# Kernel optimization log

Measured on AMD Instinct MI355X. Metric: run time of the kernel, lower is better.

Reference implementation:

```python
import jax, jax.numpy as jnp
import numpy as np

K = -1.0          # manifold curvature (hyperbolic / Poincare ball)
SK = 1.0          # sqrt(|K|)
EPS = 1e-7


def _artan_k(x):
    # inverse of tan_k for K<0: artanh(sqrt(|K|) x)/sqrt(|K|)
    return jnp.arctanh(jnp.clip(SK * x, -1.0 + EPS, 1.0 - EPS)) / SK


def _tan_k(x):
    return jnp.tanh(SK * x) / SK


def _norm(x):
    return jnp.maximum(jnp.linalg.norm(x, axis=-1, keepdims=True), 1e-15)


def mobius_add(x, y):
    xy = jnp.sum(x * y, -1, keepdims=True)
    x2 = jnp.sum(x * x, -1, keepdims=True)
    y2 = jnp.sum(y * y, -1, keepdims=True)
    num = (1.0 - 2.0 * K * xy - K * y2) * x + (1.0 + K * x2) * y
    den = 1.0 - 2.0 * K * xy + K * K * x2 * y2
    return num / jnp.maximum(den, 1e-15)


def mobius_scalar_mul(r, x):
    # r may be scalar or (n,1) per-row scalar
    xn = _norm(x)
    return _tan_k(r * _artan_k(xn)) * x / xn


def mobius_matvec(W, x):
    # geoopt convention: (m @ x) per point -> x @ W^T
    xn = _norm(x)
    mx = x @ W.T
    mxn = _norm(mx)
    return _tan_k(mxn / xn * _artan_k(xn)) * mx / mxn


def lambda_x(x):
    # conformal factor lambda_x = 2 / (1 + K |x|^2); returns shape (...,)
    return 2.0 / jnp.maximum(1.0 + K * jnp.sum(x * x, -1), 1e-10)


def expmap0(u):
    un = _norm(u)
    return _tan_k(un) * u / un


def logmap0(y):
    yn = _norm(y)
    return _artan_k(yn) * y / yn


def kappa_left_multiply(A, X):
    # Vectorized per-node weighted gyro-midpoint + mobius scalar mul.
    # out_i = (sum_j A_ij) otimes gyromidpoint(X, weights=A_i)
    gamma = lambda_x(X)                              # (n,)
    denom = A @ (gamma - 1.0)                        # (n,)
    denom = jnp.where(jnp.abs(denom) < 1e-10, 1e-10, denom)
    nom = A @ (gamma[:, None] * X)                   # (n,d)
    two_mean = nom / denom[:, None]
    m = mobius_scalar_mul(0.5, two_mean)             # gyromidpoint
    return mobius_scalar_mul(jnp.sum(A, axis=1, keepdims=True), m)


def setup_inputs() -> dict:
    key = jax.random.key(0)
    k1, k2, k3, k4, k5 = jax.random.split(key, 5)
    n, d, c = 8192, 256, 16
    # node embeddings on the Poincare ball (small norm, well inside the ball)
    X = 0.01 * jax.random.normal(k1, (n, d), jnp.float32)
    # dense normalized adjacency (positive weights, row sums O(1))
    A_hat = jax.random.uniform(k2, (n, n), dtype=jnp.float32) / n
    W = jax.random.uniform(k3, (d, d), dtype=jnp.float32)        # torch.rand init
    W_logits = jax.random.uniform(k4, (d, c), dtype=jnp.float32)
    # p_ks = expmap0(rand), scaled for numerical stability
    p_ks = expmap0(0.05 * jax.random.uniform(k5, (c, d), dtype=jnp.float32))
    return {"X": X, "A_hat": A_hat, "W": W, "W_logits": W_logits, "p_ks": p_ks}


def reference(X, A_hat, W, W_logits, p_ks):
    # hidden kappa-GCN layer
    XW = mobius_matvec(W, X)                          # (n,d)
    AXW = kappa_left_multiply(A_hat, XW)              # (n,d)
    H1 = expmap0(jax.nn.relu(logmap0(AXW)))           # manifold.apply(relu)
    # hyperbolic logits (kappa != 0 branch, K<0 -> asinh)
    z = mobius_add(-p_ks[None, :, :], H1[:, None, :]) # (n,k,d)
    z_n = jnp.linalg.norm(z, axis=-1)                 # (n,k)
    a_n = jnp.maximum(jnp.linalg.norm(W_logits, axis=0), 1e-15)  # (k,)
    za = jnp.einsum('nkd,dk->nk', z, W_logits)
    den = jnp.maximum(1.0 + K * z_n * z_n, 1e-10) * a_n
    dist = jnp.arcsinh(2.0 * SK * za / den)
    lam = lambda_x(p_ks)                              # (k,)
    logits = (lam * a_n / SK) * dist                  # (n,k)
    return A_hat @ logits
```

## Files before the change

### kernel.cpp

```cpp
#include <hip/hip_runtime.h>
#include <math.h>

#define Nn 8192
#define Dd 256
#define Cc 16

#define OFF_BP   4194304u
#define OFF_LOG  5242880u
#define OFF_G1B  5373952u
#define OFF_DEN  5378048u
#define OFF_RS   5410816u
#define OFF_KC   5443584u
#define OFF_LB   5443648u
#define WS_FLOATS 5509184u

typedef short vshort8 __attribute__((ext_vector_type(8)));
typedef float vfloat4 __attribute__((ext_vector_type(4)));

#define AS1 __attribute__((address_space(1)))
#define AS3 __attribute__((address_space(3)))

__device__ __forceinline__ float clip1(float x) {
    return fminf(fmaxf(x, -1.0f + 1e-7f), 1.0f - 1e-7f);
}

__device__ __forceinline__ unsigned short f2bf(float f) {
    unsigned int u = __float_as_uint(f);
    u += 0x7fff + ((u >> 16) & 1);
    return (unsigned short)(u >> 16);
}

__device__ __forceinline__ float bf2f(unsigned short b) {
    return __uint_as_float(((unsigned int)b) << 16);
}

__device__ __forceinline__ float waveReduce(float v) {
    #pragma unroll
    for (int off = 32; off; off >>= 1) v += __shfl_down(v, off);
    return v;
}

__device__ __forceinline__ float blockReduceBcast(float v, float* red) {
    int t = threadIdx.x, w = t >> 6, l = t & 63;
    v = waveReduce(v);
    if (l == 0) red[w] = v;
    __syncthreads();
    if (t == 0) red[0] = red[0] + red[1] + red[2] + red[3];
    __syncthreads();
    float r = red[0];
    __syncthreads();
    return r;
}

__global__ __launch_bounds__(256) void k_consts(const float* __restrict__ Wl,
                                                const float* __restrict__ Pk,
                                                float* __restrict__ kc) {
    __shared__ float red[8];
    int t = threadIdx.x, k = blockIdx.x;
    float pv = Pk[k * Dd + t];
    float wv = Wl[t * Cc + k];
    float p2 = blockReduceBcast(pv * pv, red);
    float pw = blockReduceBcast(pv * wv, red);
    float w2 = blockReduceBcast(wv * wv, red);
    if (t == 0) {
        float an  = fmaxf(sqrtf(w2), 1e-15f);
        float lam = 2.0f / fmaxf(1.0f - p2, 1e-10f);
        kc[k * 4 + 0] = p2; kc[k * 4 + 1] = pw;
        kc[k * 4 + 2] = an; kc[k * 4 + 3] = lam;
    }
}

__global__ __launch_bounds__(256) void k_front(const float* __restrict__ X,
                                               const float* __restrict__ W,
                                               unsigned short* __restrict__ Bp,
                                               unsigned short* __restrict__ g1b) {
    __shared__ __align__(16) unsigned short Xs[32][256];
    __shared__ __align__(16) unsigned short Gs[32][258];
    __shared__ float xs2[32];
    __shared__ float scal[32];
    __shared__ float red4[32][4];

    const int t = threadIdx.x;
    const int l = t & 63, w = t >> 6;
    const int ll = l & 15, kh = l >> 4;
    const int m0 = blockIdx.x * 32;
    const int ar = t >> 3, aq = t & 7;
    const int c0 = w * 64;

    float x2p = 0.f;
    #pragma unroll
    for (int tc = 0; tc < 4; ++tc) {
        const float* xp = &X[(size_t)(m0 + ar) * Dd + tc * 64 + aq * 8];
        vfloat4 v0 = *(const vfloat4*)xp;
        vfloat4 v1 = *(const vfloat4*)(xp + 4);
        vshort8 o;
        #pragma unroll
        for (int e = 0; e < 4; ++e) {
            x2p += v0[e] * v0[e] + v1[e] * v1[e];
            o[e] = (short)f2bf(v0[e]);
            o[e + 4] = (short)f2bf(v1[e]);
        }
        int byte = (tc * 64 + aq * 8) * 2;
        *(vshort8*)((char*)&Xs[ar][0] + (byte ^ ((ar & 7) << 4))) = o;
    }
    x2p += __shfl_xor(x2p, 1); x2p += __shfl_xor(x2p, 2); x2p += __shfl_xor(x2p, 4);
    if (aq == 0) xs2[ar] = x2p;
    __syncthreads();

    vfloat4 acc[2][4];
    #pragma unroll
    for (int mi = 0; mi < 2; ++mi)
        #pragma unroll
        for (int ni = 0; ni < 4; ++ni)
            acc[mi][ni] = (vfloat4){0.f, 0.f, 0.f, 0.f};
    #pragma unroll
    for (int tc = 0; tc < 4; ++tc) {
        vshort8 bf[8];
        #pragma unroll
        for (int ni = 0; ni < 4; ++ni)
            #pragma unroll
            for (int kk = 0; kk < 2; ++kk) {
                const float* wp = &W[(size_t)(c0 + ni * 16 + ll) * Dd
                                     + tc * 64 + kh * 8 + kk * 32];
                vfloat4 b0 = *(const vfloat4*)wp;
                vfloat4 b1 = *(const vfloat4*)(wp + 4);
                vshort8 o;
                #pragma unroll
                for (int e = 0; e < 4; ++e) {
                    o[e] = (short)f2bf(b0[e]);
                    o[e + 4] = (short)f2bf(b1[e]);
                }
                bf[ni * 2 + kk] = o;
            }
        #pragma unroll
        for (int kk = 0; kk < 2; ++kk) {
            int byte = (tc * 64 + kh * 8 + kk * 32) * 2;
            vshort8 af[2];
            #pragma unroll
            for (int mi = 0; mi < 2; ++mi) {
                int row = mi * 16 + ll;
                af[mi] = *(const vshort8*)((const char*)&Xs[row][0]
                                           + (byte ^ ((row & 7) << 4)));
            }
            #pragma unroll
            for (int mi = 0; mi < 2; ++mi)
                #pragma unroll
                for (int ni = 0; ni < 4; ++ni)
                    acc[mi][ni] = __builtin_amdgcn_mfma_f32_16x16x32_bf16(
                        af[mi], bf[ni * 2 + kk], acc[mi][ni], 0, 0, 0);
        }
    }

    #pragma unroll
    for (int mi = 0; mi < 2; ++mi)
        #pragma unroll
        for (int j = 0; j < 4; ++j) {
            float p = 0.f;
            #pragma unroll
            for (int ni = 0; ni < 4; ++ni)
                p += acc[mi][ni][j] * acc[mi][ni][j];
            p += __shfl_xor(p, 1); p += __shfl_xor(p, 2);
            p += __shfl_xor(p, 4); p += __shfl_xor(p, 8);
            if (ll == 0) red4[mi * 16 + kh * 4 + j][w] = p;
        }
    __syncthreads();

    if (t < 32) {
        float mx2 = red4[t][0] + red4[t][1] + red4[t][2] + red4[t][3];
        float xn = fmaxf(sqrtf(xs2[t]), 1e-15f);
        float mxn = fmaxf(sqrtf(mx2), 1e-15f);
        float s = tanhf(mxn / xn * atanhf(clip1(xn))) / mxn;
        float xw2 = s * s * mx2;
        float gamma = 2.0f / fmaxf(1.0f - xw2, 1e-10f);
        scal[t] = gamma * s;
        g1b[m0 + t] = f2bf(gamma - 1.0f);
    }
    __syncthreads();

    #pragma unroll
    for (int mi = 0; mi < 2; ++mi)
        #pragma unroll
        for (int ni = 0; ni < 4; ++ni) {
            int row = mi * 16 + kh * 4;
            int col = c0 + ni * 16 + ll;
            #pragma unroll
            for (int j = 0; j < 4; ++j)
                Gs[row + j][col] = f2bf(scal[row + j] * acc[mi][ni][j]);
        }
    __syncthreads();

    const int s = blockIdx.x;
    #pragma unroll
    for (int pass = 0; pass < 4; ++pass) {
        int c = pass * 256 + t;
        int gni = c >> 6, lc = c & 63;
        int col = (gni >> 2) * 64 + (gni & 3) * 16 + (lc & 15);
        int kh8 = (lc >> 4) * 8;
        vshort8 o;
        #pragma unroll
        for (int e = 0; e < 8; ++e) o[e] = (short)Gs[kh8 + e][col];
        *(vshort8*)&Bp[((size_t)(s * 16 + gni) * 64 + lc) * 8] = o;
    }
}

__device__ __forceinline__ void g2_issueB(const unsigned short* __restrict__ Bp,
        unsigned short (&BsB)[16][512], int splt, int slab, int w, int l) {
    #pragma unroll
    for (int ni = 0; ni < 4; ++ni)
        __builtin_amdgcn_global_load_lds(
            (const AS1 unsigned int*)
                (Bp + ((size_t)((splt * 64 + slab) * 16 + w * 4 + ni) * 512) + l * 8),
            (AS3 unsigned int*)&BsB[w * 4 + ni][0], 16, 0, 0);
}

__device__ __forceinline__ void g2_loadA(const float* __restrict__ Abase,
                                         int tile, float (&a8)[8]) {
    const vfloat4* p = (const vfloat4*)(Abase + tile * 32);
    *(vfloat4*)&a8[0] = p[0];
    *(vfloat4*)&a8[4] = p[1];
}

__device__ __forceinline__ void g2_stage(unsigned short (&AsB)[2048],
        const unsigned short* g1s, const float (&a8)[8],
        int tile, int rowst, int kq, float& dacc, float& racc) {
    vshort8 gv = *(const vshort8*)&g1s[tile * 32 + kq * 8];
    vshort8 o;
    #pragma unroll
    for (int e = 0; e < 8; ++e) {
        float av = a8[e];
        o[e] = (short)f2bf(av);
        dacc += av * bf2f((unsigned short)gv[e]);
        racc += av;
    }
    *(vshort8*)((char*)&AsB[0] + rowst * 64 + ((kq * 16) ^ ((rowst & 3) << 4))) = o;
}

__device__ __forceinline__ void g2_mfma(const unsigned short (&AsB)[2048],
        const unsigned short (&BsB)[16][512], int w, int kh, int ll15, int l,
        vfloat4 (&acc)[4][4]) {
    vshort8 bf[4], af[4];
    #pragma unroll
    for (int ni = 0; ni < 4; ++ni)
        bf[ni] = *(const vshort8*)&BsB[w * 4 + ni][l * 8];
    #pragma unroll
    for (int mi = 0; mi < 4; ++mi) {
        int row = mi * 16 + ll15;
        af[mi] = *(const vshort8*)((const char*)&AsB[0]
                  + row * 64 + ((kh * 16) ^ ((row & 3) << 4)));
    }
    __builtin_amdgcn_s_setprio(1);
    #pragma unroll
    for (int mi = 0; mi < 4; ++mi)
        #pragma unroll
        for (int ni = 0; ni < 4; ++ni)
            acc[mi][ni] = __builtin_amdgcn_mfma_f32_16x16x32_bf16(
                af[mi], bf[ni], acc[mi][ni], 0, 0, 0);
    __builtin_amdgcn_s_setprio(0);
}

__global__ __launch_bounds__(256, 2) void k_gemm1_mfma(
        const float* __restrict__ A,
        const unsigned short* __restrict__ Bp,
        const unsigned short* __restrict__ g1b,
        unsigned short* __restrict__ Pp,
        float* __restrict__ denp,
        float* __restrict__ rsp) {
    __shared__ __align__(16) unsigned short As[2][2048];
    __shared__ __align__(16) unsigned short Bs[4][16][512];
    __shared__ __align__(16) unsigned short g1s[2048];

    const int t = threadIdx.x, l = t & 63, w = t >> 6;
    const int id = blockIdx.x;
    const int splt = id & 3;
    const int m0 = (id >> 2) * 64;
    const int kb = splt * 2048;
    const int kh = l >> 4, ll15 = l & 15;
    const int rowst = t >> 2, kq = t & 3;

    const float* Abase = &A[(size_t)(m0 + rowst) * Nn + kb + kq * 8];

    vfloat4 acc[4][4];
    #pragma unroll
    for (int mi = 0; mi < 4; ++mi)
        #pragma unroll
        for (int ni = 0; ni < 4; ++ni)
            acc[mi][ni] = (vfloat4){0.f, 0.f, 0.f, 0.f};
    float dacc = 0.f, racc = 0.f;
    float a0[8], a1[8], a2[8], a3[8];

    uint4 g1v = *(const uint4*)&g1b[kb + t * 8];
    g2_issueB(Bp, Bs[0], splt, 0, w, l);
    g2_issueB(Bp, Bs[1], splt, 1, w, l);
    g2_issueB(Bp, Bs[2], splt, 2, w, l);
    g2_loadA(Abase, 0, a0);
    g2_loadA(Abase, 1, a1);
    g2_loadA(Abase, 2, a2);
    g2_loadA(Abase, 3, a3);
    asm volatile("s_waitcnt vmcnt(0)" ::: "memory");
    *(uint4*)&g1s[t * 8] = g1v;
    asm volatile("s_waitcnt lgkmcnt(0)" ::: "memory");
    __builtin_amdgcn_s_barrier();
    g2_stage(As[0], g1s, a0, 0, rowst, kq, dacc, racc);
    asm volatile("s_waitcnt lgkmcnt(0)" ::: "memory");
    __builtin_amdgcn_s_barrier();
    __builtin_amdgcn_sched_barrier(0);

    for (int u = 0; u < 16; ++u) {
        #pragma unroll
        for (int pp = 0; pp < 4; ++pp) {
            const int q = u * 4 + pp;
            g2_issueB(Bp, Bs[(pp + 3) & 3], splt, (q + 3) & 63, w, l);
            {
                float (&adst)[8] = (pp == 0) ? a0 : (pp == 1) ? a1
                                 : (pp == 2) ? a2 : a3;
                g2_loadA(Abase, (q + 4) & 63, adst);
            }
            asm volatile("s_waitcnt vmcnt(18)" ::: "memory");
            if (q < 63) {
                float (&asrc)[8] = (pp == 0) ? a1 : (pp == 1) ? a2
                                 : (pp == 2) ? a3 : a0;
                g2_stage(As[(q + 1) & 1], g1s, asrc, q + 1, rowst, kq, dacc, racc);
            }
            g2_mfma(As[q & 1], Bs[pp & 3], w, kh, ll15, l, acc);
            asm volatile("s_waitcnt lgkmcnt(0)" ::: "memory");
            __builtin_amdgcn_s_barrier();
            __builtin_amdgcn_sched_barrier(0);
        }
    }

    dacc += __shfl_xor(dacc, 1); dacc += __shfl_xor(dacc, 2);
    racc += __shfl_xor(racc, 1); racc += __shfl_xor(racc, 2);
    if (kq == 0) {
        denp[splt * Nn + m0 + rowst] = dacc;
        rsp [splt * Nn + m0 + rowst] = racc;
    }

    unsigned short* P = Pp + (size_t)splt * ((size_t)Nn * Dd);
    #pragma unroll
    for (int mi = 0; mi < 4; ++mi)
        #pragma unroll
        for (int ni = 0; ni < 4; ++ni) {
            int row = m0 + mi * 16 + (kh << 2);
            int col = w * 64 + ni * 16 + ll15;
            #pragma unroll
            for (int j = 0; j < 4; ++j)
                P[(size_t)(row + j) * Dd + col] = f2bf(acc[mi][ni][j]);
        }
}

__global__ __launch_bounds__(256) void k_rowfix(const unsigned short* __restrict__ Pp,
                                                const float* __restrict__ denp,
                                                const float* __restrict__ rsp,
                                                const float* __restrict__ Pk,
                                                const float* __restrict__ Wl,
                                                const float* __restrict__ kc,
                                                float* __restrict__ logits) {
    __shared__ float red[8];
    __shared__ float hs[256];
    __shared__ float PQ[16][2];
    int i = blockIdx.x, t = threadIdx.x;
    float nom = 0.f;
    #pragma unroll
    for (int s = 0; s < 4; ++s)
        nom += bf2f(Pp[(size_t)s * Nn * Dd + (size_t)i * Dd + t]);
    float dv = denp[i] + denp[Nn + i] + denp[2 * Nn + i] + denp[3 * Nn + i];
    dv = (fabsf(dv) < 1e-10f) ? 1e-10f : dv;
    float tm = nom / dv;
    float r2 = blockReduceBcast(tm * tm, red);
    float r = fmaxf(sqrtf(r2), 1e-15f);
    float mmul = tanhf(0.5f * atanhf(clip1(r))) / r;
    float mj = mmul * tm;
    float mn2 = blockReduceBcast(mj * mj, red);
    float mn = fmaxf(sqrtf(mn2), 1e-15f);
    float sA = rsp[i] + rsp[Nn + i] + rsp[2 * Nn + i] + rsp[3 * Nn + i];
    float axmul = tanhf(sA * atanhf(clip1(mn))) / mn;
    float axw = axmul * mj;
    float yn2 = blockReduceBcast(axw * axw, red);
    float yn = fmaxf(sqrtf(yn2), 1e-15f);
    float v = atanhf(clip1(yn)) / yn * axw;
    float u = fmaxf(v, 0.0f);
    float un2 = blockReduceBcast(u * u, red);
    float un = fmaxf(sqrtf(un2), 1e-15f);
    float h = tanhf(un) / un * u;
    float h2 = blockReduceBcast(h * h, red);
    hs[t] = h;
    __syncthreads();
    int w = t >> 6, l = t & 63;
    #pragma unroll
    for (int kk = 0; kk < 4; ++kk) {
        int k = w * 4 + kk;
        float pp = 0.f, qq = 0.f;
        #pragma unroll
        for (int m = 0; m < 4; ++m) {
            float hv = hs[l + 64 * m];
            pp += hv * Pk[k * Dd + l + 64 * m];
            qq += hv * Wl[(l + 64 * m) * Cc + k];
        }
        pp = waveReduce(pp);
        qq = waveReduce(qq);
        if (l == 0) { PQ[k][0] = pp; PQ[k][1] = qq; }
    }
    __syncthreads();
    if (t < 16) {
        int k = t;
        float p2 = kc[k * 4 + 0], pw = kc[k * 4 + 1];
        float an = kc[k * 4 + 2], lam = kc[k * 4 + 3];
        float P = PQ[k][0], Q = PQ[k][1];
        float alpha = 1.0f - 2.0f * P + h2;
        float beta  = 1.0f - p2;
        float Dm = fmaxf(1.0f - 2.0f * P + p2 * h2, 1e-15f);
        float za  = (-alpha * pw + beta * Q) / Dm;
        float zn2 = (alpha * alpha * p2 - 2.0f * alpha * beta * P + beta * beta * h2)
                    / (Dm * Dm);
        float dd = fmaxf(1.0f - zn2, 1e-10f) * an;
        float dist = asinhf(2.0f * za / dd);
        logits[(size_t)i * Cc + k] = lam * an * dist;
    }
}

__global__ __launch_bounds__(64) void k_packL(const float* __restrict__ L,
                                              unsigned short* __restrict__ Lb) {
    int kt = blockIdx.x;
    int l = threadIdx.x;
    vshort8 o;
    #pragma unroll
    for (int e = 0; e < 8; ++e)
        o[e] = (short)f2bf(L[(size_t)(kt * 32 + (l >> 4) * 8 + e) * Cc + (l & 15)]);
    *(vshort8*)&Lb[(size_t)kt * 512 + l * 8] = o;
}

__global__ __launch_bounds__(256, 4) void k_gemm2_mfma(
        const float* __restrict__ A,
        const unsigned short* __restrict__ Lb,
        float* __restrict__ part) {
    const int t = threadIdx.x, l = t & 63, w = t >> 6;
    const int id = blockIdx.x;
    const int splt = id & 7;
    const int m0 = (id >> 3) * 64;
    const int kb = splt * 1024;
    const int kh = l >> 4, ll15 = l & 15;
    const int r0 = m0 + w * 16;

    const float* Ab = &A[(size_t)(r0 + ll15) * Nn + kb + kh * 8];
    const unsigned short* Lbb = &Lb[(size_t)(splt * 32) * 512 + l * 8];

    vfloat4 acc = (vfloat4){0.f, 0.f, 0.f, 0.f};
    float a0[8], a1[8], a2[8], a3[8];
    vshort8 b0, b1, b2, b3;

    *(vfloat4*)&a0[0] = *(const vfloat4*)(Ab);
    *(vfloat4*)&a0[4] = *(const vfloat4*)(Ab + 4);
    b0 = *(const vshort8*)(Lbb);
    *(vfloat4*)&a1[0] = *(const vfloat4*)(Ab + 32);
    *(vfloat4*)&a1[4] = *(const vfloat4*)(Ab + 36);
    b1 = *(const vshort8*)(Lbb + 512);
    *(vfloat4*)&a2[0] = *(const vfloat4*)(Ab + 64);
    *(vfloat4*)&a2[4] = *(const vfloat4*)(Ab + 68);
    b2 = *(const vshort8*)(Lbb + 1024);

    for (int u = 0; u < 8; ++u) {
        #pragma unroll
        for (int pp = 0; pp < 4; ++pp) {
            const int kt = u * 4 + pp;
            if (kt < 29) {
                float (&adst)[8] = (pp == 0) ? a3 : (pp == 1) ? a0
                                 : (pp == 2) ? a1 : a2;
                vshort8& bdst = (pp == 0) ? b3 : (pp == 1) ? b0
                              : (pp == 2) ? b1 : b2;
                *(vfloat4*)&adst[0] = *(const vfloat4*)(Ab + (kt + 3) * 32);
                *(vfloat4*)&adst[4] = *(const vfloat4*)(Ab + (kt + 3) * 32 + 4);
                bdst = *(const vshort8*)(Lbb + (kt + 3) * 512);
            }
            float (&acur)[8] = (pp == 0) ? a0 : (pp == 1) ? a1
                             : (pp == 2) ? a2 : a3;
            vshort8& bcur = (pp == 0) ? b0 : (pp == 1) ? b1
                          : (pp == 2) ? b2 : b3;
            vshort8 af;
            #pragma unroll
            for (int e = 0; e < 8; ++e) af[e] = (short)f2bf(acur[e]);
            acc = __builtin_amdgcn_mfma_f32_16x16x32_bf16(af, bcur, acc, 0, 0, 0);
        }
    }

    float* P = part + (size_t)splt * ((size_t)Nn * Cc);
    #pragma unroll
    for (int j = 0; j < 4; ++j)
        P[(size_t)(r0 + kh * 4 + j) * Cc + ll15] = acc[j];
}

__global__ __launch_bounds__(256) void k_reduce(const float* __restrict__ part,
                                                float* __restrict__ out) {
    int i = blockIdx.x * 256 + threadIdx.x;
    float s = 0.f;
    #pragma unroll
    for (int j = 0; j < 8; ++j) s += part[(size_t)j * (Nn * Cc) + i];
    out[i] = s;
}

extern "C" void kernel_launch(void* const* d_in, const int* in_sizes, int n_in,
                              void* d_out, int out_size, void* d_ws, size_t ws_size,
                              hipStream_t stream) {
    const float* X  = (const float*)d_in[0];
    const float* A  = (const float*)d_in[1];
    const float* W  = (const float*)d_in[2];
    const float* Wl = (const float*)d_in[3];
    const float* Pk = (const float*)d_in[4];
    float* out = (float*)d_out;
    float* ws = (float*)d_ws;
    if (ws_size < (size_t)WS_FLOATS * sizeof(float)) return;

    unsigned short* Pp  = (unsigned short*)ws;
    float* part = ws;
    unsigned short* Bp  = (unsigned short*)(ws + OFF_BP);
    float* lg   = ws + OFF_LOG;
    unsigned short* g1b = (unsigned short*)(ws + OFF_G1B);
    float* denp = ws + OFF_DEN;
    float* rsp  = ws + OFF_RS;
    float* kc   = ws + OFF_KC;
    unsigned short* Lbp = (unsigned short*)(ws + OFF_LB);

    k_consts<<<16, 256, 0, stream>>>(Wl, Pk, kc);
    k_front<<<256, 256, 0, stream>>>(X, W, Bp, g1b);
    k_gemm1_mfma<<<512, 256, 0, stream>>>(A, Bp, g1b, Pp, denp, rsp);
    k_rowfix<<<Nn, 256, 0, stream>>>(Pp, denp, rsp, Pk, Wl, kc, lg);
    k_packL<<<256, 64, 0, stream>>>(lg, Lbp);
    k_gemm2_mfma<<<1024, 256, 0, stream>>>(A, Lbp, part);
    k_reduce<<<512, 256, 0, stream>>>(part, out);
}
```

Before: 210.1 us.

## Restructure A_hat GEMM to register-only per-wave tiles without LDS staging

The split-K MFMA GEMM over the dense adjacency is rewritten so that each wave owns 16 rows and all 256 output columns. A and B fragments are loaded straight from global memory into registers with a two-stage register double buffer, which removes the LDS staging, swizzling and per-step block barriers. The cost is that every wave re-reads the full B slab from global or L2 instead of sharing it through LDS, and register pressure rises with 16 accumulators plus two 16-entry B fragment buffers. This may lower occupancy or cause spills.

```diff
diff --git a/kernel.cpp b/kernel.cpp
--- a/kernel.cpp
+++ b/kernel.cpp
@@ -16,9 +16,6 @@
 
 typedef short vshort8 __attribute__((ext_vector_type(8)));
 typedef float vfloat4 __attribute__((ext_vector_type(4)));
-
-#define AS1 __attribute__((address_space(1)))
-#define AS3 __attribute__((address_space(3)))
 
 __device__ __forceinline__ float clip1(float x) {
     return fminf(fmaxf(x, -1.0f + 1e-7f), 1.0f - 1e-7f);
@@ -203,61 +200,6 @@
     }
 }
 
-__device__ __forceinline__ void g2_issueB(const unsigned short* __restrict__ Bp,
-        unsigned short (&BsB)[16][512], int splt, int slab, int w, int l) {
-    #pragma unroll
-    for (int ni = 0; ni < 4; ++ni)
-        __builtin_amdgcn_global_load_lds(
-            (const AS1 unsigned int*)
-                (Bp + ((size_t)((splt * 64 + slab) * 16 + w * 4 + ni) * 512) + l * 8),
-            (AS3 unsigned int*)&BsB[w * 4 + ni][0], 16, 0, 0);
-}
-
-__device__ __forceinline__ void g2_loadA(const float* __restrict__ Abase,
-                                         int tile, float (&a8)[8]) {
-    const vfloat4* p = (const vfloat4*)(Abase + tile * 32);
-    *(vfloat4*)&a8[0] = p[0];
-    *(vfloat4*)&a8[4] = p[1];
-}
-
-__device__ __forceinline__ void g2_stage(unsigned short (&AsB)[2048],
-        const unsigned short* g1s, const float (&a8)[8],
-        int tile, int rowst, int kq, float& dacc, float& racc) {
-    vshort8 gv = *(const vshort8*)&g1s[tile * 32 + kq * 8];
-    vshort8 o;
-    #pragma unroll
-    for (int e = 0; e < 8; ++e) {
-        float av = a8[e];
-        o[e] = (short)f2bf(av);
-        dacc += av * bf2f((unsigned short)gv[e]);
-        racc += av;
-    }
-    *(vshort8*)((char*)&AsB[0] + rowst * 64 + ((kq * 16) ^ ((rowst & 3) << 4))) = o;
-}
-
-__device__ __forceinline__ void g2_mfma(const unsigned short (&AsB)[2048],
-        const unsigned short (&BsB)[16][512], int w, int kh, int ll15, int l,
-        vfloat4 (&acc)[4][4]) {
-    vshort8 bf[4], af[4];
-    #pragma unroll
-    for (int ni = 0; ni < 4; ++ni)
-        bf[ni] = *(const vshort8*)&BsB[w * 4 + ni][l * 8];
-    #pragma unroll
-    for (int mi = 0; mi < 4; ++mi) {
-        int row = mi * 16 + ll15;
-        af[mi] = *(const vshort8*)((const char*)&AsB[0]
-                  + row * 64 + ((kh * 16) ^ ((row & 3) << 4)));
-    }
-    __builtin_amdgcn_s_setprio(1);
-    #pragma unroll
-    for (int mi = 0; mi < 4; ++mi)
-        #pragma unroll
-        for (int ni = 0; ni < 4; ++ni)
-            acc[mi][ni] = __builtin_amdgcn_mfma_f32_16x16x32_bf16(
-                af[mi], bf[ni], acc[mi][ni], 0, 0, 0);
-    __builtin_amdgcn_s_setprio(0);
-}
-
 __global__ __launch_bounds__(256, 2) void k_gemm1_mfma(
         const float* __restrict__ A,
         const unsigned short* __restrict__ Bp,
@@ -265,87 +207,103 @@
         unsigned short* __restrict__ Pp,
         float* __restrict__ denp,
         float* __restrict__ rsp) {
-    __shared__ __align__(16) unsigned short As[2][2048];
-    __shared__ __align__(16) unsigned short Bs[4][16][512];
-    __shared__ __align__(16) unsigned short g1s[2048];
-
     const int t = threadIdx.x, l = t & 63, w = t >> 6;
     const int id = blockIdx.x;
     const int splt = id & 3;
-    const int m0 = (id >> 2) * 64;
+    const int r0 = (id >> 2) * 64 + w * 16;
     const int kb = splt * 2048;
     const int kh = l >> 4, ll15 = l & 15;
-    const int rowst = t >> 2, kq = t & 3;
-
-    const float* Abase = &A[(size_t)(m0 + rowst) * Nn + kb + kq * 8];
-
-    vfloat4 acc[4][4];
-    #pragma unroll
-    for (int mi = 0; mi < 4; ++mi)
-        #pragma unroll
-        for (int ni = 0; ni < 4; ++ni)
-            acc[mi][ni] = (vfloat4){0.f, 0.f, 0.f, 0.f};
+
+    const float* Ab = &A[(size_t)(r0 + ll15) * Nn + kb + kh * 8];
+    const unsigned short* Bb = Bp + (size_t)(splt * 64) * 8192 + l * 8;
+    const unsigned short* g1p = g1b + kb + kh * 8;
+
+    vfloat4 acc[16];
+    #pragma unroll
+    for (int gni = 0; gni < 16; ++gni)
+        acc[gni] = (vfloat4){0.f, 0.f, 0.f, 0.f};
     float dacc = 0.f, racc = 0.f;
-    float a0[8], a1[8], a2[8], a3[8];
-
-    uint4 g1v = *(const uint4*)&g1b[kb + t * 8];
-    g2_issueB(Bp, Bs[0], splt, 0, w, l);
-    g2_issueB(Bp, Bs[1], splt, 1, w, l);
-    g2_issueB(Bp, Bs[2], splt, 2, w, l);
-    g2_loadA(Abase, 0, a0);
-    g2_loadA(Abase, 1, a1);
-    g2_loadA(Abase, 2, a2);
-    g2_loadA(Abase, 3, a3);
-    asm volatile("s_waitcnt vmcnt(0)" ::: "memory");
-    *(uint4*)&g1s[t * 8] = g1v;
-    asm volatile("s_waitcnt lgkmcnt(0)" ::: "memory");
-    __builtin_amdgcn_s_barrier();
-    g2_stage(As[0], g1s, a0, 0, rowst, kq, dacc, racc);
-    asm volatile("s_waitcnt lgkmcnt(0)" ::: "memory");
-    __builtin_amdgcn_s_barrier();
-    __builtin_amdgcn_sched_barrier(0);
-
-    for (int u = 0; u < 16; ++u) {
-        #pragma unroll
-        for (int pp = 0; pp < 4; ++pp) {
-            const int q = u * 4 + pp;
-            g2_issueB(Bp, Bs[(pp + 3) & 3], splt, (q + 3) & 63, w, l);
+
+    vshort8 bf0[16], bf1[16];
+    float a0[8], a1[8];
+    vshort8 g10, g11;
+
+    #pragma unroll
+    for (int gni = 0; gni < 16; ++gni)
+        bf0[gni] = *(const vshort8*)(Bb + gni * 512);
+    {
+        const vfloat4* p = (const vfloat4*)(Ab);
+        *(vfloat4*)&a0[0] = p[0];
+        *(vfloat4*)&a0[4] = p[1];
+    }
+    g10 = *(const vshort8*)(g1p);
+
+    for (int u = 0; u < 32; ++u) {
+        {
+            const int kt = 2 * u;
+            #pragma unroll
+            for (int gni = 0; gni < 16; ++gni)
+                bf1[gni] = *(const vshort8*)(Bb + (kt + 1) * 8192 + gni * 512);
             {
-                float (&adst)[8] = (pp == 0) ? a0 : (pp == 1) ? a1
-                                 : (pp == 2) ? a2 : a3;
-                g2_loadA(Abase, (q + 4) & 63, adst);
-            }
-            asm volatile("s_waitcnt vmcnt(18)" ::: "memory");
-            if (q < 63) {
-                float (&asrc)[8] = (pp == 0) ? a1 : (pp == 1) ? a2
-                                 : (pp == 2) ? a3 : a0;
-                g2_stage(As[(q + 1) & 1], g1s, asrc, q + 1, rowst, kq, dacc, racc);
-            }
-            g2_mfma(As[q & 1], Bs[pp & 3], w, kh, ll15, l, acc);
-            asm volatile("s_waitcnt lgkmcnt(0)" ::: "memory");
-            __builtin_amdgcn_s_barrier();
-            __builtin_amdgcn_sched_barrier(0);
-        }
-    }
-
-    dacc += __shfl_xor(dacc, 1); dacc += __shfl_xor(dacc, 2);
-    racc += __shfl_xor(racc, 1); racc += __shfl_xor(racc, 2);
-    if (kq == 0) {
-        denp[splt * Nn + m0 + rowst] = dacc;
-        rsp [splt * Nn + m0 + rowst] = racc;
+                const vfloat4* p = (const vfloat4*)(Ab + (kt + 1) * 32);
+                *(vfloat4*)&a1[0] = p[0];
+                *(vfloat4*)&a1[4] = p[1];
+            }
+            g11 = *(const vshort8*)(g1p + (kt + 1) * 32);
+            vshort8 af;
+            #pragma unroll
+            for (int e = 0; e < 8; ++e) {
+                float av = a0[e];
+                af[e] = (short)f2bf(av);
+                dacc += av * bf2f((unsigned short)g10[e]);
+                racc += av;
+            }
+            #pragma unroll
+            for (int gni = 0; gni < 16; ++gni)
+                acc[gni] = __builtin_amdgcn_mfma_f32_16x16x32_bf16(
+                    af, bf0[gni], acc[gni], 0, 0, 0);
+        }
+        {
+            const int kt = 2 * u + 1;
+            if (kt + 1 < 64) {
+                #pragma unroll
+                for (int gni = 0; gni < 16; ++gni)
+                    bf0[gni] = *(const vshort8*)(Bb + (kt + 1) * 8192 + gni * 512);
+                const vfloat4* p = (const vfloat4*)(Ab + (kt + 1) * 32);
+                *(vfloat4*)&a0[0] = p[0];
+                *(vfloat4*)&a0[4] = p[1];
+                g10 = *(const vshort8*)(g1p + (kt + 1) * 32);
+            }
+            vshort8 af;
+            #pragma unroll
+            for (int e = 0; e < 8; ++e) {
+                float av = a1[e];
+                af[e] = (short)f2bf(av);
+                dacc += av * bf2f((unsigned short)g11[e]);
+                racc += av;
+            }
+            #pragma unroll
+            for (int gni = 0; gni < 16; ++gni)
+                acc[gni] = __builtin_amdgcn_mfma_f32_16x16x32_bf16(
+                    af, bf1[gni], acc[gni], 0, 0, 0);
+        }
+    }
+
+    dacc += __shfl_xor(dacc, 16); dacc += __shfl_xor(dacc, 32);
+    racc += __shfl_xor(racc, 16); racc += __shfl_xor(racc, 32);
+    if (l < 16) {
+        denp[splt * Nn + r0 + l] = dacc;
+        rsp [splt * Nn + r0 + l] = racc;
     }
 
     unsigned short* P = Pp + (size_t)splt * ((size_t)Nn * Dd);
     #pragma unroll
-    for (int mi = 0; mi < 4; ++mi)
-        #pragma unroll
-        for (int ni = 0; ni < 4; ++ni) {
-            int row = m0 + mi * 16 + (kh << 2);
-            int col = w * 64 + ni * 16 + ll15;
-            #pragma unroll
-            for (int j = 0; j < 4; ++j)
-                P[(size_t)(row + j) * Dd + col] = f2bf(acc[mi][ni][j]);
-        }
+    for (int gni = 0; gni < 16; ++gni) {
+        int col = (gni >> 2) * 64 + (gni & 3) * 16 + ll15;
+        #pragma unroll
+        for (int j = 0; j < 4; ++j)
+            P[(size_t)(r0 + kh * 4 + j) * Dd + col] = f2bf(acc[gni][j]);
+    }
 }
 
 __global__ __launch_bounds__(256) void k_rowfix(const unsigned short* __restrict__ Pp,
```

Result: slower. 282.7 us (+34.6%).
